# Kernel tuning notes

Measured on AMD Instinct MI355X. Metric: run time of the kernel, lower is better.

The kernel has to match this reference:

```python
import jax, jax.numpy as jnp
import numpy as np

B, T, H = 16, 512, 2048


def setup_inputs() -> dict:
    key = jax.random.key(0)
    kx, kw, kb = jax.random.split(key, 3)
    x = jax.random.normal(kx, (B, T, H), dtype=jnp.float32)
    # scale like nn.Linear default init so the linear recurrence is stable over T steps
    W = jax.random.normal(kw, (H, 2 * H), dtype=jnp.float32) / jnp.sqrt(2.0 * H)
    b = jax.random.normal(kb, (H,), dtype=jnp.float32) * 0.01
    return {"x": x, "W": W, "b": b}


def reference(x, W, b):
    # torch: h_t = Linear([x_t ; h_{t-1}]) = [x_t ; h_{t-1}] @ W.T + b
    # split W (H, 2H) into Wx (H, H) acting on x and Wh (H, H) acting on h
    Hh = x.shape[-1]
    Wx, Wh = W[:, :Hh], W[:, Hh:]
    # hoist the input projection out of the recurrence: one big GEMM
    u = jnp.einsum('bth,gh->btg', x, Wx) + b  # (B, T, H)
    h0 = jnp.zeros((x.shape[0], Hh), dtype=x.dtype)

    def step(h, u_t):
        h = u_t + h @ Wh.T  # affine recurrence, no nonlinearity (matches source)
        return h, h

    h_last, outs = jax.lax.scan(step, h0, jnp.swapaxes(u, 0, 1))  # outs: (T, B, H)
    out = jnp.swapaxes(outs, 0, 1)  # (B, T, H), batch_first
    return out, h_last
```

## Files before the change

kernel.cpp:

```cpp
#include <hip/hip_runtime.h>
#include <hip/hip_fp16.h>
#include <stdint.h>

#define HDIM 2048
#define BATCH 16
#define TLEN 512
#define TH   1048576
#define OUT_MAIN 16777216

using floatx4 = __attribute__((ext_vector_type(4))) float;
using shortx8 = __attribute__((ext_vector_type(8))) short;
using halfx8  = __attribute__((ext_vector_type(8))) _Float16;
typedef unsigned long long ull;

static __device__ __forceinline__ unsigned f16bits(float f) {
    _Float16 h = (_Float16)f;
    return (unsigned)*(unsigned short*)&h;
}

__global__ void cast_x_kernel(const float* __restrict__ x, _Float16* __restrict__ xh, int n) {
    int i = blockIdx.x * blockDim.x + threadIdx.x;
    int stride = gridDim.x * blockDim.x;
    for (; i < n; i += stride) xh[i] = (_Float16)x[i];
}

__global__ void cast_w_kernel(const float* __restrict__ W,
                              _Float16* __restrict__ wxh,
                              _Float16* __restrict__ whh) {
    int i = blockIdx.x * blockDim.x + threadIdx.x;
    int stride = gridDim.x * blockDim.x;
    for (; i < HDIM * HDIM; i += stride) {
        int g = i >> 11, k = i & (HDIM - 1);
        wxh[i] = (_Float16)W[g * (2 * HDIM) + k];
        whh[i] = (_Float16)W[g * (2 * HDIM) + HDIM + k];
    }
}

__global__ void transpose_wh_kernel(const float* __restrict__ W,
                                    _Float16* __restrict__ whT) {
    __shared__ float tile[32][33];
    int bx = blockIdx.x * 32, by = blockIdx.y * 32;
    int tx = threadIdx.x, ty = threadIdx.y;
#pragma unroll
    for (int r = 0; r < 32; r += 8)
        tile[ty + r][tx] = W[(size_t)(by + ty + r) * (2 * HDIM) + HDIM + bx + tx];
    __syncthreads();
#pragma unroll
    for (int r = 0; r < 32; r += 8)
        whT[(size_t)(bx + ty + r) * HDIM + by + tx] = (_Float16)tile[tx][ty + r];
}

__global__ __launch_bounds__(256) void gemm_u_kernel(
    const _Float16* __restrict__ xh,
    const _Float16* __restrict__ wxh,
    const float* __restrict__ bias,
    float* __restrict__ out,
    _Float16* __restrict__ uh)
{
    __shared__ __align__(16) short As[4 * 128 * 8];
    __shared__ __align__(16) short Bs[4 * 128 * 8];

    const int j = threadIdx.x;
    const int m0 = blockIdx.x * 128;
    const int n0 = blockIdx.y * 128;
    const int w = j >> 6, lane = j & 63;
    const int wm = (w >> 1) * 64, wn = (w & 1) * 64;
    const int quad = lane >> 4, l15 = lane & 15;

    const int mA0 = j & 127, kg0 = j >> 7;
    const int mA1 = (j + 256) & 127, kg1 = (j + 256) >> 7;

    floatx4 acc[4][4] = {};

    shortx8 ra0 = *(const shortx8*)(xh  + (size_t)(m0 + mA0) * HDIM + kg0 * 8);
    shortx8 ra1 = *(const shortx8*)(xh  + (size_t)(m0 + mA1) * HDIM + kg1 * 8);
    shortx8 rb0 = *(const shortx8*)(wxh + (size_t)(n0 + mA0) * HDIM + kg0 * 8);
    shortx8 rb1 = *(const shortx8*)(wxh + (size_t)(n0 + mA1) * HDIM + kg1 * 8);

    for (int kt = 0; kt < 64; ++kt) {
        ((shortx8*)As)[kg0 * 128 + mA0] = ra0;
        ((shortx8*)As)[kg1 * 128 + mA1] = ra1;
        ((shortx8*)Bs)[kg0 * 128 + mA0] = rb0;
        ((shortx8*)Bs)[kg1 * 128 + mA1] = rb1;
        __syncthreads();

        if (kt < 63) {
            int k = (kt + 1) * 32;
            ra0 = *(const shortx8*)(xh  + (size_t)(m0 + mA0) * HDIM + k + kg0 * 8);
            ra1 = *(const shortx8*)(xh  + (size_t)(m0 + mA1) * HDIM + k + kg1 * 8);
            rb0 = *(const shortx8*)(wxh + (size_t)(n0 + mA0) * HDIM + k + kg0 * 8);
            rb1 = *(const shortx8*)(wxh + (size_t)(n0 + mA1) * HDIM + k + kg1 * 8);
        }

        halfx8 af[4], bf[4];
#pragma unroll
        for (int mt = 0; mt < 4; ++mt)
            af[mt] = ((const halfx8*)As)[quad * 128 + wm + mt * 16 + l15];
#pragma unroll
        for (int nt = 0; nt < 4; ++nt)
            bf[nt] = ((const halfx8*)Bs)[quad * 128 + wn + nt * 16 + l15];
#pragma unroll
        for (int mt = 0; mt < 4; ++mt)
#pragma unroll
            for (int nt = 0; nt < 4; ++nt)
                acc[mt][nt] = __builtin_amdgcn_mfma_f32_16x16x32_f16(af[mt], bf[nt], acc[mt][nt], 0, 0, 0);
        __syncthreads();
    }

#pragma unroll
    for (int nt = 0; nt < 4; ++nt) {
        int gn = n0 + wn + nt * 16 + l15;
        float bv = bias[gn];
#pragma unroll
        for (int mt = 0; mt < 4; ++mt) {
#pragma unroll
            for (int r = 0; r < 4; ++r) {
                int gm = m0 + wm + mt * 16 + quad * 4 + r;
                float v = acc[mt][nt][r] + bv;
                out[(size_t)gm * HDIM + gn] = v;
                uh[(size_t)gm * HDIM + gn] = (_Float16)v;
            }
        }
    }
}

__global__ __launch_bounds__(256) void gemm_w2_kernel(
    const _Float16* __restrict__ whh,
    const _Float16* __restrict__ wT,
    _Float16* __restrict__ w2)
{
    __shared__ __align__(16) short As[4 * 128 * 8];
    __shared__ __align__(16) short Bs[4 * 128 * 8];

    const int j = threadIdx.x;
    const int m0 = blockIdx.x * 128;
    const int n0 = blockIdx.y * 128;
    const int w = j >> 6, lane = j & 63;
    const int wm = (w >> 1) * 64, wn = (w & 1) * 64;
    const int quad = lane >> 4, l15 = lane & 15;

    const int mA0 = j & 127, kg0 = j >> 7;
    const int mA1 = (j + 256) & 127, kg1 = (j + 256) >> 7;

    floatx4 acc[4][4] = {};

    shortx8 ra0 = *(const shortx8*)(whh + (size_t)(m0 + mA0) * HDIM + kg0 * 8);
    shortx8 ra1 = *(const shortx8*)(whh + (size_t)(m0 + mA1) * HDIM + kg1 * 8);
    shortx8 rb0 = *(const shortx8*)(wT  + (size_t)(n0 + mA0) * HDIM + kg0 * 8);
    shortx8 rb1 = *(const shortx8*)(wT  + (size_t)(n0 + mA1) * HDIM + kg1 * 8);

    for (int kt = 0; kt < 64; ++kt) {
        ((shortx8*)As)[kg0 * 128 + mA0] = ra0;
        ((shortx8*)As)[kg1 * 128 + mA1] = ra1;
        ((shortx8*)Bs)[kg0 * 128 + mA0] = rb0;
        ((shortx8*)Bs)[kg1 * 128 + mA1] = rb1;
        __syncthreads();

        if (kt < 63) {
            int k = (kt + 1) * 32;
            ra0 = *(const shortx8*)(whh + (size_t)(m0 + mA0) * HDIM + k + kg0 * 8);
            ra1 = *(const shortx8*)(whh + (size_t)(m0 + mA1) * HDIM + k + kg1 * 8);
            rb0 = *(const shortx8*)(wT  + (size_t)(n0 + mA0) * HDIM + k + kg0 * 8);
            rb1 = *(const shortx8*)(wT  + (size_t)(n0 + mA1) * HDIM + k + kg1 * 8);
        }

        halfx8 af[4], bf[4];
#pragma unroll
        for (int mt = 0; mt < 4; ++mt)
            af[mt] = ((const halfx8*)As)[quad * 128 + wm + mt * 16 + l15];
#pragma unroll
        for (int nt = 0; nt < 4; ++nt)
            bf[nt] = ((const halfx8*)Bs)[quad * 128 + wn + nt * 16 + l15];
#pragma unroll
        for (int mt = 0; mt < 4; ++mt)
#pragma unroll
            for (int nt = 0; nt < 4; ++nt)
                acc[mt][nt] = __builtin_amdgcn_mfma_f32_16x16x32_f16(af[mt], bf[nt], acc[mt][nt], 0, 0, 0);
        __syncthreads();
    }

#pragma unroll
    for (int nt = 0; nt < 4; ++nt) {
        int gn = n0 + wn + nt * 16 + l15;
#pragma unroll
        for (int mt = 0; mt < 4; ++mt)
#pragma unroll
            for (int r = 0; r < 4; ++r) {
                int gm = m0 + wm + mt * 16 + quad * 4 + r;
                w2[(size_t)gm * HDIM + gn] = (_Float16)acc[mt][nt][r];
            }
    }
}

__global__ __launch_bounds__(256) void gemm_v_kernel(
    const _Float16* __restrict__ uh,
    const _Float16* __restrict__ whh,
    float* __restrict__ out)
{
    __shared__ __align__(16) short As[4 * 128 * 8];
    __shared__ __align__(16) short Bs[4 * 128 * 8];

    const int j = threadIdx.x;
    const int m0 = blockIdx.x * 128;
    const int n0 = blockIdx.y * 128;
    const int w = j >> 6, lane = j & 63;
    const int wm = (w >> 1) * 64, wn = (w & 1) * 64;
    const int quad = lane >> 4, l15 = lane & 15;

    const int mA0 = j & 127, kg0 = j >> 7;
    const int mA1 = (j + 256) & 127, kg1 = (j + 256) >> 7;

    int rowA0 = m0 + mA0 - 1; if (rowA0 < 0) rowA0 = 0;
    int rowA1 = m0 + mA1 - 1; if (rowA1 < 0) rowA1 = 0;

    floatx4 acc[4][4] = {};

    shortx8 ra0 = *(const shortx8*)(uh  + (size_t)rowA0 * HDIM + kg0 * 8);
    shortx8 ra1 = *(const shortx8*)(uh  + (size_t)rowA1 * HDIM + kg1 * 8);
    shortx8 rb0 = *(const shortx8*)(whh + (size_t)(n0 + mA0) * HDIM + kg0 * 8);
    shortx8 rb1 = *(const shortx8*)(whh + (size_t)(n0 + mA1) * HDIM + kg1 * 8);

    for (int kt = 0; kt < 64; ++kt) {
        ((shortx8*)As)[kg0 * 128 + mA0] = ra0;
        ((shortx8*)As)[kg1 * 128 + mA1] = ra1;
        ((shortx8*)Bs)[kg0 * 128 + mA0] = rb0;
        ((shortx8*)Bs)[kg1 * 128 + mA1] = rb1;
        __syncthreads();

        if (kt < 63) {
            int k = (kt + 1) * 32;
            ra0 = *(const shortx8*)(uh  + (size_t)rowA0 * HDIM + k + kg0 * 8);
            ra1 = *(const shortx8*)(uh  + (size_t)rowA1 * HDIM + k + kg1 * 8);
            rb0 = *(const shortx8*)(whh + (size_t)(n0 + mA0) * HDIM + k + kg0 * 8);
            rb1 = *(const shortx8*)(whh + (size_t)(n0 + mA1) * HDIM + k + kg1 * 8);
        }

        halfx8 af[4], bf[4];
#pragma unroll
        for (int mt = 0; mt < 4; ++mt)
            af[mt] = ((const halfx8*)As)[quad * 128 + wm + mt * 16 + l15];
#pragma unroll
        for (int nt = 0; nt < 4; ++nt)
            bf[nt] = ((const halfx8*)Bs)[quad * 128 + wn + nt * 16 + l15];
#pragma unroll
        for (int mt = 0; mt < 4; ++mt)
#pragma unroll
            for (int nt = 0; nt < 4; ++nt)
                acc[mt][nt] = __builtin_amdgcn_mfma_f32_16x16x32_f16(af[mt], bf[nt], acc[mt][nt], 0, 0, 0);
        __syncthreads();
    }

#pragma unroll
    for (int nt = 0; nt < 4; ++nt) {
        int gn = n0 + wn + nt * 16 + l15;
#pragma unroll
        for (int mt = 0; mt < 4; ++mt)
#pragma unroll
            for (int r = 0; r < 4; ++r) {
                int gm = m0 + wm + mt * 16 + quad * 4 + r;
                float uval = out[(size_t)gm * HDIM + gn];
                float res = ((gm & 511) == 0) ? uval : (acc[mt][nt][r] + uval);
                out[(size_t)gm * HDIM + gn] = res;
            }
    }
}

__global__ __launch_bounds__(512) void rnn_scan_kernel(
    const _Float16* __restrict__ w2,
    short* __restrict__ ring,
    float* __restrict__ out,
    unsigned* __restrict__ flags)
{
    __shared__ float ps[8 * 2 * 16 * 17];

    const int j = threadIdx.x;
    const int w = j >> 6, lane = j & 63;
    const int quad = lane >> 4, l15 = lane & 15;
    const int chain = blockIdx.x & 1;
    const int rank = blockIdx.x >> 1;
    const int n0 = rank * 32;

    unsigned* myflag = flags + (chain * 64 + rank) * 32;
    const unsigned* pollbase = flags + chain * 64 * 32;

    halfx8 af[2][8];
#pragma unroll
    for (int gt = 0; gt < 2; ++gt)
#pragma unroll
        for (int c = 0; c < 8; ++c) {
            int row = n0 + gt * 16 + l15;
            int k = w * 256 + c * 32 + quad * 8;
            af[gt][c] = *(const halfx8*)(w2 + (size_t)row * HDIM + k);
        }

    const int rn = j & 31, rb = j >> 5;
    const int gt_r = rn >> 4, row_r = rn & 15;

    for (int s = 0; s < 256; ++s) {
        const int t = chain + 2 * s;
        short* slot_next = ring + (size_t)(s * 2 + chain) * 32768;

        float uv = out[(size_t)rb * TH + (size_t)t * HDIM + n0 + rn];

        floatx4 acc[2][2] = {};
        if (s > 0) {
            const short* slot_prev = ring + (size_t)((s - 1) * 2 + chain) * 32768;
            if (lane < 8) {
                const unsigned* fp = pollbase + (w * 8 + lane) * 32;
                while (__hip_atomic_load(fp, __ATOMIC_RELAXED, __HIP_MEMORY_SCOPE_AGENT) < (unsigned)s) {}
            }
            __asm__ __volatile__("" ::: "memory");

#pragma unroll
            for (int c = 0; c < 8; ++c) {
                int kg = w * 32 + c * 4 + quad;
                halfx8 bh = *(const halfx8*)(slot_prev + kg * 128 + l15 * 8);
                int cp = c & 1;
                acc[0][cp] = __builtin_amdgcn_mfma_f32_16x16x32_f16(af[0][c], bh, acc[0][cp], 0, 0, 0);
                acc[1][cp] = __builtin_amdgcn_mfma_f32_16x16x32_f16(af[1][c], bh, acc[1][cp], 0, 0, 0);
            }
        }

        floatx4 a0 = acc[0][0] + acc[0][1];
        floatx4 a1 = acc[1][0] + acc[1][1];
#pragma unroll
        for (int r = 0; r < 4; ++r) {
            ps[((w * 2 + 0) * 16 + quad * 4 + r) * 17 + l15] = a0[r];
            ps[((w * 2 + 1) * 16 + quad * 4 + r) * 17 + l15] = a1[r];
        }
        __syncthreads();

        float sv_f = uv;
#pragma unroll
        for (int ww = 0; ww < 8; ++ww)
            sv_f += ps[((ww * 2 + gt_r) * 16 + row_r) * 17 + rb];

        int n = n0 + rn;

        unsigned hb = f16bits(sv_f);
        unsigned hb2 = __shfl_down(hb, 1);
        if ((j & 1) == 0) {
            int idx = (n >> 3) * 128 + rb * 8 + (n & 7);
            __hip_atomic_store((unsigned*)(slot_next + idx), hb | (hb2 << 16),
                               __ATOMIC_RELAXED, __HIP_MEMORY_SCOPE_AGENT);
        }

        __syncthreads();
        if (j == 0)
            __hip_atomic_store(myflag, (unsigned)(s + 1), __ATOMIC_RELAXED, __HIP_MEMORY_SCOPE_AGENT);

        out[(size_t)rb * TH + (size_t)t * HDIM + n] = sv_f;
        if (t == TLEN - 1) out[(size_t)OUT_MAIN + (size_t)rb * HDIM + n] = sv_f;
    }
}

extern "C" void kernel_launch(void* const* d_in, const int* in_sizes, int n_in,
                              void* d_out, int out_size, void* d_ws, size_t ws_size,
                              hipStream_t stream) {
    (void)in_sizes; (void)n_in; (void)out_size; (void)ws_size;
    const float* x    = (const float*)d_in[0];
    const float* W    = (const float*)d_in[1];
    const float* bias = (const float*)d_in[2];
    float* out = (float*)d_out;
    char* ws = (char*)d_ws;

    _Float16* xh  = (_Float16*)(ws);
    _Float16* whT = (_Float16*)(ws);
    _Float16* w2  = (_Float16*)(ws + 8388608);
    short*    ring = (short*)(ws + 16777216);
    _Float16* wxh = (_Float16*)(ws + 33554432);
    _Float16* whh = (_Float16*)(ws + 41943040);
    _Float16* uh  = (_Float16*)(ws + 50331648);
    unsigned* flags = (unsigned*)(ws + 83886080);

    hipMemsetAsync(ws + 83886080, 0, 16384, stream);

    cast_x_kernel<<<8192, 256, 0, stream>>>(x, xh, OUT_MAIN);
    cast_w_kernel<<<8192, 256, 0, stream>>>(W, wxh, whh);
    gemm_u_kernel<<<dim3(64, 16), 256, 0, stream>>>(xh, wxh, bias, out, uh);
    transpose_wh_kernel<<<dim3(64, 64), dim3(32, 8), 0, stream>>>(W, whT);
    gemm_v_kernel<<<dim3(64, 16), 256, 0, stream>>>(uh, whh, out);
    gemm_w2_kernel<<<dim3(16, 16), 256, 0, stream>>>(whh, whT, w2);
    rnn_scan_kernel<<<128, 512, 0, stream>>>(w2, ring, out, flags);
}
```

Measured before the change: 1.007 ms.

## Use per-wave flags and double-buffered LDS to drop the second block barrier

```diff
diff --git a/kernel.cpp b/kernel.cpp
--- a/kernel.cpp
+++ b/kernel.cpp
@@ -271,7 +271,7 @@
     float* __restrict__ out,
     unsigned* __restrict__ flags)
 {
-    __shared__ float ps[8 * 2 * 16 * 17];
+    __shared__ float ps[2][8 * 2 * 16 * 17];
 
     const int j = threadIdx.x;
     const int w = j >> 6, lane = j & 63;
@@ -280,8 +280,8 @@
     const int rank = blockIdx.x >> 1;
     const int n0 = rank * 32;
 
-    unsigned* myflag = flags + (chain * 64 + rank) * 32;
-    const unsigned* pollbase = flags + chain * 64 * 32;
+    unsigned* myflag = flags + (((chain * 64 + rank) * 8) + w) * 32;
+    const unsigned* mypoll = flags + ((chain * 64 + (w * 8 + (lane >> 3))) * 8 + (lane & 7)) * 32;
 
     halfx8 af[2][8];
 #pragma unroll
@@ -305,9 +305,9 @@
         floatx4 acc[2][2] = {};
         if (s > 0) {
             const short* slot_prev = ring + (size_t)((s - 1) * 2 + chain) * 32768;
-            if (lane < 8) {
-                const unsigned* fp = pollbase + (w * 8 + lane) * 32;
-                while (__hip_atomic_load(fp, __ATOMIC_RELAXED, __HIP_MEMORY_SCOPE_AGENT) < (unsigned)s) {}
+            for (;;) {
+                unsigned f = __hip_atomic_load(mypoll, __ATOMIC_RELAXED, __HIP_MEMORY_SCOPE_AGENT);
+                if (__all((int)(f >= (unsigned)s))) break;
             }
             __asm__ __volatile__("" ::: "memory");
 
@@ -323,33 +323,36 @@
 
         floatx4 a0 = acc[0][0] + acc[0][1];
         floatx4 a1 = acc[1][0] + acc[1][1];
+        float* psb = ps[s & 1];
 #pragma unroll
         for (int r = 0; r < 4; ++r) {
-            ps[((w * 2 + 0) * 16 + quad * 4 + r) * 17 + l15] = a0[r];
-            ps[((w * 2 + 1) * 16 + quad * 4 + r) * 17 + l15] = a1[r];
+            psb[((w * 2 + 0) * 16 + quad * 4 + r) * 17 + l15] = a0[r];
+            psb[((w * 2 + 1) * 16 + quad * 4 + r) * 17 + l15] = a1[r];
         }
         __syncthreads();
 
         float sv_f = uv;
 #pragma unroll
         for (int ww = 0; ww < 8; ++ww)
-            sv_f += ps[((ww * 2 + gt_r) * 16 + row_r) * 17 + rb];
+            sv_f += psb[((ww * 2 + gt_r) * 16 + row_r) * 17 + rb];
 
         int n = n0 + rn;
 
         unsigned hb = f16bits(sv_f);
-        unsigned hb2 = __shfl_down(hb, 1);
-        if ((j & 1) == 0) {
+        unsigned h1 = __shfl_down(hb, 1);
+        unsigned h2 = __shfl_down(hb, 2);
+        unsigned h3 = __shfl_down(hb, 3);
+        if ((j & 3) == 0) {
             int idx = (n >> 3) * 128 + rb * 8 + (n & 7);
-            __hip_atomic_store((unsigned*)(slot_next + idx), hb | (hb2 << 16),
+            ull pk = (ull)(hb | (h1 << 16)) | (((ull)(h2 | (h3 << 16))) << 32);
+            __hip_atomic_store((ull*)(slot_next + idx), pk,
                                __ATOMIC_RELAXED, __HIP_MEMORY_SCOPE_AGENT);
         }
-
-        __syncthreads();
-        if (j == 0)
+        out[(size_t)rb * TH + (size_t)t * HDIM + n] = sv_f;
+        __asm__ __volatile__("s_waitcnt vmcnt(1)" ::: "memory");
+        if (lane == 0)
             __hip_atomic_store(myflag, (unsigned)(s + 1), __ATOMIC_RELAXED, __HIP_MEMORY_SCOPE_AGENT);
 
-        out[(size_t)rb * TH + (size_t)t * HDIM + n] = sv_f;
         if (t == TLEN - 1) out[(size_t)OUT_MAIN + (size_t)rb * HDIM + n] = sv_f;
     }
 }
@@ -373,7 +376,7 @@
     _Float16* uh  = (_Float16*)(ws + 50331648);
     unsigned* flags = (unsigned*)(ws + 83886080);
 
-    hipMemsetAsync(ws + 83886080, 0, 16384, stream);
+    hipMemsetAsync(ws + 83886080, 0, 131072, stream);
 
     cast_x_kernel<<<8192, 256, 0, stream>>>(x, xh, OUT_MAIN);
     cast_w_kernel<<<8192, 256, 0, stream>>>(W, wxh, whh);
```

Result: slower. 1.310 ms (+30.1%).
